# Performance work log

Hardware: AMD Instinct MI355X
Metric: run time of the kernel (lower is better)

## Reference

```python
import jax, jax.numpy as jnp
import numpy as np

N = 200000          # number of points (max_num_points // 2)
GRID = 0.4          # voxel edge length (meters)
NUM_BATCH = 4       # number of scenes encoded in points[:, 0]


def setup_inputs() -> dict:
    key = jax.random.key(0)
    k1, k2 = jax.random.split(key)
    xyz = jax.random.uniform(k1, (N, 3), minval=-50.0, maxval=50.0, dtype=jnp.float32)
    b = jax.random.randint(k2, (N,), 0, NUM_BATCH).astype(jnp.float32)
    points = jnp.concatenate([b[:, None], xyz], axis=1)  # [N, 4] = (batch, x, y, z)
    return {"points": points}


def reference(points):
    n = points.shape[0]
    vs = jnp.array([1.0, GRID, GRID, GRID], dtype=points.dtype)  # voxel_size
    decay2 = jnp.sum(vs[1:] ** 2) / 4.0  # decay_radius**2 = (||voxel_size||/2)**2

    pc_min = points.min(0) - vs * 2.0
    pc_max = points.max(0) + vs * 2.0
    coors = jnp.round((points - pc_min) / vs).astype(jnp.int32) + 1   # [N,4] voxel coords
    dims = (jnp.round((pc_max - pc_min) / vs) + 3.0).astype(jnp.int32)  # [4]

    def flatten(c):  # 4-D voxel coordinate -> 1-D hash key
        f = c[..., 0]
        for i in range(1, 4):
            f = f * dims[i] + c[..., i]
        return f

    keys = flatten(coors)  # [N]
    # unique occupied voxels (= query voxels); pad with max key so array stays sorted
    uq = jnp.unique(keys, size=n, fill_value=keys.max())  # [N] sorted
    valid = jnp.concatenate([jnp.array([True]), uq[1:] != uq[:-1]])  # first occurrence only

    # 27 spatial neighbor offsets ([0,-1,-1,-1]..[0,1,1,1]); batch offset is 0
    r = jnp.arange(-1, 2, dtype=jnp.int32)
    off = jnp.stack(jnp.meshgrid(r, r, r, indexing="ij"), -1).reshape(-1, 3)  # [27,3]
    off4 = jnp.concatenate([jnp.zeros((27, 1), jnp.int32), off], axis=1)      # [27,4]

    nb = coors[:, None, :] + off4[None, :, :]   # [N,27,4]: each point scatters to 27 query voxels
    nkeys = flatten(nb)                          # [N,27]
    idx = jnp.clip(jnp.searchsorted(uq, nkeys), 0, n - 1)
    hit = uq[idx] == nkeys                       # query voxel exists (is occupied)
    idx_safe = jnp.where(hit, idx, 0)

    # distance-decayed weight of point w.r.t. the query voxel center
    ctr = (nb[..., 1:].astype(points.dtype) - 1.0) * vs[1:] + pc_min[1:]  # [N,27,3]
    d2 = jnp.sum((points[:, None, 1:] - ctr) ** 2, axis=-1)               # [N,27]
    w = jnp.where(hit, jnp.exp(-d2 / decay2), 0.0)

    seg = lambda data: jax.ops.segment_sum(data, idx_safe.reshape(-1), num_segments=n)
    wf = w.reshape(-1)                               # [N*27]
    wsum = seg(wf)                                   # [M]
    p_rep = jnp.broadcast_to(points[:, None, :], (n, 27, 4)).reshape(-1, 4)
    wp = seg(wf[:, None] * p_rep)                    # [M,4] weighted first moment
    outer = points[:, 1:, None] * points[:, None, 1:]  # [N,3,3] xyz second moment
    o_rep = jnp.broadcast_to(outer[:, None], (n, 27, 3, 3)).reshape(-1, 3, 3)
    wo = seg(wf[:, None, None] * o_rep)              # [M,3,3]

    ok = valid & (wsum > 0)
    ws = jnp.where(ok, wsum, 1.0)
    mu = wp / ws[:, None]                            # [M,4] weighted mean (batch,x,y,z)
    sigma = wo / ws[:, None, None] - mu[:, 1:, None] * mu[:, None, 1:]  # weighted covariance
    sigma = (sigma + jnp.swapaxes(sigma, 1, 2)) / 2.0
    # padded / empty slots: well-conditioned placeholder with distinct singular values
    base = jnp.diag(jnp.array([3.0, 2.0, 1.0], dtype=points.dtype))
    sigma = jnp.where(ok[:, None, None], sigma, base)

    U, S, _ = jnp.linalg.svd(sigma)
    S = jnp.maximum(jnp.sqrt(S), 1e-6)
    flip = jnp.linalg.det(U) < 0
    col = jnp.where(flip, -1.0, 1.0)
    scale = jnp.stack([jnp.ones_like(col), jnp.ones_like(col), col], axis=-1)  # flip 3rd column
    R = (U * scale[:, None, :]) * S[:, None, :]

    mu = mu * ok[:, None]
    R = R * ok[:, None, None]
    return mu, R
```

## Files before the change

kernel.cpp:

```cpp
#include <hip/hip_runtime.h>
#include <stdint.h>


#define WMAX   5402624u
#define PBLK   2638
#define CHUNK  11
#define HCAP   1024
#define HITCAP 786432
#define MMB    784

struct Hdr {
  float pc_min[4];
  int   dims[4];
  int   M;
};

__device__ __forceinline__ unsigned fkey_map(float f) {
  unsigned u = __float_as_uint(f);
  return (u & 0x80000000u) ? ~u : (u | 0x80000000u);
}
__device__ __forceinline__ float fkey_unmap(unsigned u) {
  unsigned b = (u & 0x80000000u) ? (u ^ 0x80000000u) : ~u;
  return __uint_as_float(b);
}

__device__ __forceinline__ void coors_from(float4 p, float pc0, float pc1,
                                           float pc2, float pc3, int c[4]) {
  c[0] = (int)rintf((p.x - pc0) / 1.0f) + 1;
  c[1] = (int)rintf((p.y - pc1) / 0.4f) + 1;
  c[2] = (int)rintf((p.z - pc2) / 0.4f) + 1;
  c[3] = (int)rintf((p.w - pc3) / 0.4f) + 1;
}

__device__ __forceinline__ void direct_accum(float* __restrict__ acc, int r,
                                             float wgt, float4 p) {
  float* a = acc + (size_t)r * 12;
  atomicAdd((unsigned*)(a + 11), 1u);
  atomicAdd(a + 0, wgt);
  atomicAdd(a + 1, wgt * p.x);
  atomicAdd(a + 2, wgt * p.y);
  atomicAdd(a + 3, wgt * p.z);
  atomicAdd(a + 4, wgt * p.w);
  atomicAdd(a + 5, wgt * p.y * p.y);
  atomicAdd(a + 6, wgt * p.y * p.z);
  atomicAdd(a + 7, wgt * p.y * p.w);
  atomicAdd(a + 8, wgt * p.z * p.z);
  atomicAdd(a + 9, wgt * p.z * p.w);
  atomicAdd(a + 10, wgt * p.w * p.w);
}

__device__ __forceinline__ void jacobi_out(float ws, float4 v0, float4 v1,
                                           float4 v2, bool ok,
                                           float* mu_o, float* R_o) {
  if (!ok) {
    mu_o[0] = mu_o[1] = mu_o[2] = mu_o[3] = 0.0f;
    #pragma unroll
    for (int k = 0; k < 9; ++k) R_o[k] = 0.0f;
    return;
  }
  float mu0 = v0.y / ws, mu1 = v0.z / ws, mu2 = v0.w / ws, mu3 = v1.x / ws;
  float A[3][3];
  A[0][0] = v1.y / ws - mu1 * mu1;
  A[0][1] = A[1][0] = v1.z / ws - mu1 * mu2;
  A[0][2] = A[2][0] = v1.w / ws - mu1 * mu3;
  A[1][1] = v2.x / ws - mu2 * mu2;
  A[1][2] = A[2][1] = v2.y / ws - mu2 * mu3;
  A[2][2] = v2.z / ws - mu3 * mu3;

  float V[3][3] = {{1.f, 0.f, 0.f}, {0.f, 1.f, 0.f}, {0.f, 0.f, 1.f}};
  for (int sweep = 0; sweep < 8; ++sweep) {
    #pragma unroll
    for (int pi = 0; pi < 3; ++pi) {
      int p = (pi == 2) ? 1 : 0;
      int q = (pi == 0) ? 1 : 2;
      float apq = A[p][q];
      if (apq == 0.0f) continue;
      float app = A[p][p], aqq = A[q][q];
      float theta = (aqq - app) / (2.0f * apq);
      float t = 1.0f / (fabsf(theta) + sqrtf(theta * theta + 1.0f));
      if (theta < 0.0f) t = -t;
      float cth = 1.0f / sqrtf(t * t + 1.0f);
      float sth = t * cth;
      A[p][p] = app - t * apq;
      A[q][q] = aqq + t * apq;
      A[p][q] = A[q][p] = 0.0f;
      int k = 3 - p - q;
      float akp = A[k][p], akq = A[k][q];
      A[k][p] = A[p][k] = cth * akp - sth * akq;
      A[k][q] = A[q][k] = sth * akp + cth * akq;
      #pragma unroll
      for (int r = 0; r < 3; ++r) {
        float vp = V[r][p], vq = V[r][q];
        V[r][p] = cth * vp - sth * vq;
        V[r][q] = sth * vp + cth * vq;
      }
    }
  }
  float a[3] = {fabsf(A[0][0]), fabsf(A[1][1]), fabsf(A[2][2])};
  int idx[3] = {0, 1, 2};
  if (a[idx[0]] < a[idx[1]]) { int t = idx[0]; idx[0] = idx[1]; idx[1] = t; }
  if (a[idx[1]] < a[idx[2]]) { int t = idx[1]; idx[1] = idx[2]; idx[2] = t; }
  if (a[idx[0]] < a[idx[1]]) { int t = idx[0]; idx[0] = idx[1]; idx[1] = t; }
  float S0 = fmaxf(sqrtf(a[idx[0]]), 1e-6f);
  float S1 = fmaxf(sqrtf(a[idx[1]]), 1e-6f);
  float S2 = fmaxf(sqrtf(a[idx[2]]), 1e-6f);
  float U[3][3];
  #pragma unroll
  for (int r = 0; r < 3; ++r) {
    U[r][0] = V[r][idx[0]];
    U[r][1] = V[r][idx[1]];
    U[r][2] = V[r][idx[2]];
  }
  float det = U[0][0] * (U[1][1] * U[2][2] - U[1][2] * U[2][1])
            - U[0][1] * (U[1][0] * U[2][2] - U[1][2] * U[2][0])
            + U[0][2] * (U[1][0] * U[2][1] - U[1][1] * U[2][0]);
  float f2 = (det < 0.0f) ? -1.0f : 1.0f;
  mu_o[0] = mu0; mu_o[1] = mu1; mu_o[2] = mu2; mu_o[3] = mu3;
  R_o[0] = U[0][0] * S0; R_o[1] = U[0][1] * S1; R_o[2] = U[0][2] * S2 * f2;
  R_o[3] = U[1][0] * S0; R_o[4] = U[1][1] * S1; R_o[5] = U[1][2] * S2 * f2;
  R_o[6] = U[2][0] * S0; R_o[7] = U[2][1] * S1; R_o[8] = U[2][2] * S2 * f2;
}

__global__ void k_zero_minmax(const float4* __restrict__ pts, int n,
                              unsigned* __restrict__ mmpart,
                              unsigned* __restrict__ bm,
                              float* __restrict__ acc,
                              unsigned* __restrict__ g_cnt) {
  __shared__ unsigned smem[4 * 8];
  const int gtid = blockIdx.x * 256 + threadIdx.x;
  const int gridT = gridDim.x * 256;

  uint4 z = {0u, 0u, 0u, 0u};
  uint4* bm4 = (uint4*)bm;
  for (int i = gtid; i < (int)(WMAX / 4); i += gridT) bm4[i] = z;
  uint4* acc4 = (uint4*)acc;
  int acc4n = n * 3;
  for (int i = gtid; i < acc4n; i += gridT) acc4[i] = z;
  if (gtid == 0) *g_cnt = 0u;

  float mn[4] = { INFINITY,  INFINITY,  INFINITY,  INFINITY};
  float mx[4] = {-INFINITY, -INFINITY, -INFINITY, -INFINITY};
  for (int i = gtid; i < n; i += gridT) {
    float4 p = pts[i];
    mn[0] = fminf(mn[0], p.x); mx[0] = fmaxf(mx[0], p.x);
    mn[1] = fminf(mn[1], p.y); mx[1] = fmaxf(mx[1], p.y);
    mn[2] = fminf(mn[2], p.z); mx[2] = fmaxf(mx[2], p.z);
    mn[3] = fminf(mn[3], p.w); mx[3] = fmaxf(mx[3], p.w);
  }
  #pragma unroll
  for (int off = 32; off > 0; off >>= 1) {
    #pragma unroll
    for (int c = 0; c < 4; ++c) {
      mn[c] = fminf(mn[c], __shfl_down(mn[c], off));
      mx[c] = fmaxf(mx[c], __shfl_down(mx[c], off));
    }
  }
  int wave = threadIdx.x >> 6;
  if ((threadIdx.x & 63) == 0) {
    #pragma unroll
    for (int c = 0; c < 4; ++c) {
      smem[wave * 8 + c]     = fkey_map(mn[c]);
      smem[wave * 8 + 4 + c] = fkey_map(mx[c]);
    }
  }
  __syncthreads();
  int t = threadIdx.x;
  if (t < 8) {
    unsigned u = smem[t];
    #pragma unroll
    for (int w = 1; w < 4; ++w)
      u = (t < 4) ? min(u, smem[w * 8 + t]) : max(u, smem[w * 8 + t]);
    mmpart[blockIdx.x * 8 + t] = u;
  }
}

__global__ void k_prep(const unsigned* __restrict__ mmpart, Hdr* h, int nb) {
  __shared__ unsigned s[256 * 8];
  int t = threadIdx.x;
  unsigned v[8];
  #pragma unroll
  for (int c = 0; c < 4; ++c) { v[c] = 0xFFFFFFFFu; v[4 + c] = 0u; }
  for (int b = t; b < nb; b += 256) {
    #pragma unroll
    for (int c = 0; c < 4; ++c) {
      v[c] = min(v[c], mmpart[b * 8 + c]);
      v[4 + c] = max(v[4 + c], mmpart[b * 8 + 4 + c]);
    }
  }
  #pragma unroll
  for (int c = 0; c < 8; ++c) s[t * 8 + c] = v[c];
  __syncthreads();
  for (int off = 128; off > 0; off >>= 1) {
    if (t < off) {
      #pragma unroll
      for (int c = 0; c < 4; ++c)
        s[t * 8 + c] = min(s[t * 8 + c], s[(t + off) * 8 + c]);
      #pragma unroll
      for (int c = 4; c < 8; ++c)
        s[t * 8 + c] = max(s[t * 8 + c], s[(t + off) * 8 + c]);
    }
    __syncthreads();
  }
  if (t == 0) {
    const float vs[4] = {1.0f, 0.4f, 0.4f, 0.4f};
    #pragma unroll
    for (int c = 0; c < 4; ++c) {
      float mn = fkey_unmap(s[c]);
      float mx = fkey_unmap(s[4 + c]);
      float pmin = mn - vs[c] * 2.0f;
      float pmax = mx + vs[c] * 2.0f;
      h->pc_min[c] = pmin;
      h->dims[c] = (int)rintf((pmax - pmin) / vs[c]) + 3;
    }
  }
}

__global__ void k_mark(const float4* __restrict__ pts, int n,
                       const Hdr* __restrict__ h, unsigned* __restrict__ bm) {
  int i = blockIdx.x * 256 + threadIdx.x;
  if (i >= n) return;
  float4 p = pts[i];
  int c[4];
  coors_from(p, h->pc_min[0], h->pc_min[1], h->pc_min[2], h->pc_min[3], c);
  int key = ((c[0] * h->dims[1] + c[1]) * h->dims[2] + c[2]) * h->dims[3] + c[3];
  unsigned uk = (unsigned)key;
  if (uk >= WMAX * 32u) return;
  atomicOr(&bm[uk >> 5], 1u << (uk & 31u));
}

__global__ void k_scanA(const unsigned* __restrict__ bm,
                        unsigned short* __restrict__ rank16,
                        unsigned* __restrict__ part) {
  __shared__ unsigned s[256];
  int t = threadIdx.x;
  size_t base = (size_t)blockIdx.x * 2048 + (size_t)t * 8;
  uint4 a = *(const uint4*)(bm + base);
  uint4 b = *(const uint4*)(bm + base + 4);
  unsigned pc[8] = {(unsigned)__popc(a.x), (unsigned)__popc(a.y),
                    (unsigned)__popc(a.z), (unsigned)__popc(a.w),
                    (unsigned)__popc(b.x), (unsigned)__popc(b.y),
                    (unsigned)__popc(b.z), (unsigned)__popc(b.w)};
  unsigned sum = 0;
  #pragma unroll
  for (int k = 0; k < 8; ++k) sum += pc[k];
  s[t] = sum; __syncthreads();
  for (int off = 1; off < 256; off <<= 1) {
    unsigned v = (t >= off) ? s[t - off] : 0u;
    __syncthreads();
    s[t] += v;
    __syncthreads();
  }
  unsigned run = s[t] - sum;
  unsigned r[8];
  #pragma unroll
  for (int k = 0; k < 8; ++k) { r[k] = run; run += pc[k]; }
  uint4 o;
  o.x = (r[0] & 0xFFFFu) | (r[1] << 16);
  o.y = (r[2] & 0xFFFFu) | (r[3] << 16);
  o.z = (r[4] & 0xFFFFu) | (r[5] << 16);
  o.w = (r[6] & 0xFFFFu) | (r[7] << 16);
  *(uint4*)(rank16 + base) = o;
  if (t == 255) part[blockIdx.x] = s[255];
}

__global__ void k_scanB(unsigned* __restrict__ part, Hdr* h) {
  __shared__ unsigned s[256];
  int t = threadIdx.x;
  int lo = t * CHUNK;
  unsigned local[CHUNK];
  unsigned sum = 0;
  #pragma unroll
  for (int k = 0; k < CHUNK; ++k) {
    int j = lo + k;
    local[k] = (j < PBLK) ? part[j] : 0u;
    sum += local[k];
  }
  s[t] = sum; __syncthreads();
  for (int off = 1; off < 256; off <<= 1) {
    unsigned v = (t >= off) ? s[t - off] : 0u;
    __syncthreads();
    s[t] += v;
    __syncthreads();
  }
  unsigned run = s[t] - sum;
  #pragma unroll
  for (int k = 0; k < CHUNK; ++k) {
    int j = lo + k;
    if (j < PBLK) part[j] = run;
    run += local[k];
  }
  if (t == 255) h->M = (int)s[255];
}

__global__ void k_probe(const float4* __restrict__ pts, int n,
                        const Hdr* __restrict__ h,
                        const unsigned* __restrict__ bm,
                        const unsigned short* __restrict__ rank16,
                        const unsigned* __restrict__ part,
                        int* __restrict__ hit_i, int* __restrict__ hit_r,
                        float* __restrict__ hit_w,
                        unsigned* __restrict__ g_cnt,
                        float* __restrict__ acc) {
  __shared__ int s_cnt;
  __shared__ int s_base;
  __shared__ int   s_i[HCAP];
  __shared__ int   s_r[HCAP];
  __shared__ float s_w[HCAP];
  if (threadIdx.x == 0) s_cnt = 0;
  __syncthreads();
  int i = blockIdx.x * 256 + threadIdx.x;
  const float gg = 0.4f * 0.4f;
  const float decay2 = (gg + gg + gg) * 0.25f;
  if (i < n) {
    float4 p = pts[i];
    int c[4];
    coors_from(p, h->pc_min[0], h->pc_min[1], h->pc_min[2], h->pc_min[3], c);
    int d1 = h->dims[1], d2 = h->dims[2], d3 = h->dims[3];
    float m1 = h->pc_min[1], m2 = h->pc_min[2], m3 = h->pc_min[3];
    #pragma unroll
    for (int dx = -1; dx <= 1; ++dx) {
      #pragma unroll
      for (int dy = -1; dy <= 1; ++dy) {
        int n1 = c[1] + dx, n2 = c[2] + dy;
        int kc = ((c[0] * d1 + n1) * d2 + n2) * d3 + c[3];
        unsigned k = (unsigned)kc;
        if (k < 1u || k + 1u >= WMAX * 32u) continue;
        unsigned w = k >> 5, b = k & 31u;
        unsigned cur = bm[w];
        unsigned tri;
        if (b == 0u)
          tri = (bm[w - 1] >> 31) | ((cur & 3u) << 1);
        else if (b == 31u)
          tri = ((cur >> 30) & 3u) | ((bm[w + 1] & 1u) << 2);
        else
          tri = (cur >> (b - 1)) & 7u;
        if (!tri) continue;
        #pragma unroll
        for (int j = 0; j < 3; ++j) {
          if (!((tri >> j) & 1u)) continue;
          unsigned kj = k + (unsigned)(j - 1);
          unsigned wj = kj >> 5, bj = kj & 31u;
          unsigned word = (wj == w) ? cur : bm[wj];
          int r = (int)(part[kj >> 16] + (unsigned)rank16[wj] +
                        __popc(word & ((1u << bj) - 1u)));
          int n3 = c[3] + (j - 1);
          float cx = (float)(n1 - 1) * 0.4f + m1;
          float cy = (float)(n2 - 1) * 0.4f + m2;
          float cz = (float)(n3 - 1) * 0.4f + m3;
          float ex = p.y - cx, ey = p.z - cy, ez = p.w - cz;
          float dd = ex * ex + ey * ey + ez * ez;
          float wgt = expf(-dd / decay2);
          int pos = atomicAdd(&s_cnt, 1);
          if (pos < HCAP) {
            s_i[pos] = i; s_r[pos] = r; s_w[pos] = wgt;
          } else {
            direct_accum(acc, r, wgt, p);
          }
        }
      }
    }
  }
  __syncthreads();
  int cnt = min(s_cnt, HCAP);
  if (threadIdx.x == 0) s_base = (int)atomicAdd(g_cnt, (unsigned)cnt);
  __syncthreads();
  int base = s_base;
  for (int j = threadIdx.x; j < cnt; j += 256) {
    int gpos = base + j;
    int r = s_r[j];
    if (gpos < HITCAP) {
      hit_i[gpos] = s_i[j];
      hit_r[gpos] = r;
      hit_w[gpos] = s_w[j];
      atomicAdd((unsigned*)(acc + (size_t)r * 12 + 11), 1u);
    } else {
      direct_accum(acc, r, s_w[j], pts[s_i[j]]);
    }
  }
}

__global__ void k_drain(const float4* __restrict__ pts,
                        const int* __restrict__ hit_i,
                        const int* __restrict__ hit_r,
                        const float* __restrict__ hit_w,
                        const unsigned* __restrict__ g_cnt,
                        float* __restrict__ acc) {
  int total = min((int)*g_cnt, HITCAP);
  for (int j = blockIdx.x * 256 + threadIdx.x; j < total;
       j += gridDim.x * 256) {
    int r = hit_r[j];
    float wgt = hit_w[j];
    float4 q = pts[hit_i[j]];
    float* a = acc + (size_t)r * 12;
    unsigned c = *(const unsigned*)(a + 11);
    if (c == 1u) {
      float4 v0 = {wgt, wgt * q.x, wgt * q.y, wgt * q.z};
      float4 v1 = {wgt * q.w, wgt * q.y * q.y, wgt * q.y * q.z,
                   wgt * q.y * q.w};
      float4 v2 = {wgt * q.z * q.z, wgt * q.z * q.w, wgt * q.w * q.w, 0.0f};
      float4* av = (float4*)a;
      av[0] = v0; av[1] = v1; av[2] = v2;
    } else {
      atomicAdd(a + 0, wgt);
      atomicAdd(a + 1, wgt * q.x);
      atomicAdd(a + 2, wgt * q.y);
      atomicAdd(a + 3, wgt * q.z);
      atomicAdd(a + 4, wgt * q.w);
      atomicAdd(a + 5, wgt * q.y * q.y);
      atomicAdd(a + 6, wgt * q.y * q.z);
      atomicAdd(a + 7, wgt * q.y * q.w);
      atomicAdd(a + 8, wgt * q.z * q.z);
      atomicAdd(a + 9, wgt * q.z * q.w);
      atomicAdd(a + 10, wgt * q.w * q.w);
    }
  }
}

__global__ void k_finalize(const Hdr* __restrict__ h,
                           const float* __restrict__ acc,
                           float* __restrict__ out_mu,
                           float* __restrict__ out_R, int n) {
  int i = blockIdx.x * 256 + threadIdx.x;
  if (i >= n) return;
  const float4* av = (const float4*)(acc + (size_t)i * 12);
  float4 v0 = av[0], v1 = av[1], v2 = av[2];
  float ws = v0.x;
  bool ok = (i < h->M) && (ws > 0.0f);
  jacobi_out(ws, v0, v1, v2, ok, out_mu + (size_t)i * 4,
             out_R + (size_t)i * 9);
}

extern "C" void kernel_launch(void* const* d_in, const int* in_sizes, int n_in,
                              void* d_out, int out_size, void* d_ws,
                              size_t ws_size, hipStream_t stream) {
  const float4* pts = (const float4*)d_in[0];
  int n = in_sizes[0] / 4;
  float* out = (float*)d_out;
  float* outR = out + (size_t)4 * n;

  char* ws = (char*)d_ws;
  Hdr* hdr = (Hdr*)ws;
  size_t off = 256;
  unsigned* mmpart = (unsigned*)(ws + off);      off += (size_t)MMB * 8 * 4;
  unsigned* bm = (unsigned*)(ws + off);          off += (size_t)WMAX * 4;
  unsigned short* rank16 = (unsigned short*)(ws + off); off += (size_t)WMAX * 2;
  unsigned* part = (unsigned*)(ws + off);        off += 4096 * 4;
  unsigned* g_cnt = (unsigned*)(ws + off);       off += 256;
  int* hit_i = (int*)(ws + off);                 off += (size_t)HITCAP * 4;
  int* hit_r = (int*)(ws + off);                 off += (size_t)HITCAP * 4;
  float* hit_w = (float*)(ws + off);             off += (size_t)HITCAP * 4;
  float* acc = (float*)(ws + off);
  size_t needed = off + (size_t)n * 12 * 4;
  if (ws_size < needed) return;

  int nb = (n + 255) / 256;
  k_zero_minmax<<<MMB, 256, 0, stream>>>(pts, n, mmpart, bm, acc, g_cnt);
  k_prep<<<1, 256, 0, stream>>>(mmpart, hdr, MMB);
  k_mark<<<nb, 256, 0, stream>>>(pts, n, hdr, bm);
  k_scanA<<<PBLK, 256, 0, stream>>>(bm, rank16, part);
  k_scanB<<<1, 256, 0, stream>>>(part, hdr);
  k_probe<<<nb, 256, 0, stream>>>(pts, n, hdr, bm, rank16, part,
                                  hit_i, hit_r, hit_w, g_cnt, acc);
  k_drain<<<512, 256, 0, stream>>>(pts, hit_i, hit_r, hit_w, g_cnt, acc);
  k_finalize<<<nb, 256, 0, stream>>>(hdr, acc, out, outR, n);
}
```

Measured before the change: 176.8 us.

## Restrict bitmap zero/scan to occupied key range, add coarse occupancy bitmap, fuse scans

Computes the range of scan blocks that the batch-coordinate span can actually touch and zeroes and scans only that part of the voxel bitmap instead of the whole buffer. Adds a byte-level coarse bitmap so probes skip loads of empty bitmap words. Merges the two scan kernels with a last-block-done counter, splits min/max from zeroing, and writes the single-point voxel output directly in the drain kernel, so finalize skips those voxels. In exchange it adds an extra coarse-bitmap lookup per probe and relies on atomic completion ordering. It also changes the single-point result to mu equal to the point and R equal to 1e-6 times the identity, which may differ from the reference weighted mean.

```diff
diff --git a/kernel.cpp b/kernel.cpp
--- a/kernel.cpp
+++ b/kernel.cpp
@@ -7,12 +7,12 @@
 #define CHUNK  11
 #define HCAP   1024
 #define HITCAP 786432
-#define MMB    784
 
 struct Hdr {
   float pc_min[4];
   int   dims[4];
   int   M;
+  int   sb_lo, sb_hi;
 };
 
 __device__ __forceinline__ unsigned fkey_map(float f) {
@@ -35,7 +35,7 @@
 __device__ __forceinline__ void direct_accum(float* __restrict__ acc, int r,
                                              float wgt, float4 p) {
   float* a = acc + (size_t)r * 12;
-  atomicAdd((unsigned*)(a + 11), 1u);
+  atomicAdd((unsigned*)(a + 11), 2u);
   atomicAdd(a + 0, wgt);
   atomicAdd(a + 1, wgt * p.x);
   atomicAdd(a + 2, wgt * p.y);
@@ -50,14 +50,7 @@
 }
 
 __device__ __forceinline__ void jacobi_out(float ws, float4 v0, float4 v1,
-                                           float4 v2, bool ok,
-                                           float* mu_o, float* R_o) {
-  if (!ok) {
-    mu_o[0] = mu_o[1] = mu_o[2] = mu_o[3] = 0.0f;
-    #pragma unroll
-    for (int k = 0; k < 9; ++k) R_o[k] = 0.0f;
-    return;
-  }
+                                           float4 v2, float* mu_o, float* R_o) {
   float mu0 = v0.y / ws, mu1 = v0.z / ws, mu2 = v0.w / ws, mu3 = v1.x / ws;
   float A[3][3];
   A[0][0] = v1.y / ws - mu1 * mu1;
@@ -121,26 +114,13 @@
   R_o[6] = U[2][0] * S0; R_o[7] = U[2][1] * S1; R_o[8] = U[2][2] * S2 * f2;
 }
 
-__global__ void k_zero_minmax(const float4* __restrict__ pts, int n,
-                              unsigned* __restrict__ mmpart,
-                              unsigned* __restrict__ bm,
-                              float* __restrict__ acc,
-                              unsigned* __restrict__ g_cnt) {
+__global__ void k_minmax(const float4* __restrict__ pts, int n,
+                         unsigned* __restrict__ mmpart) {
   __shared__ unsigned smem[4 * 8];
-  const int gtid = blockIdx.x * 256 + threadIdx.x;
-  const int gridT = gridDim.x * 256;
-
-  uint4 z = {0u, 0u, 0u, 0u};
-  uint4* bm4 = (uint4*)bm;
-  for (int i = gtid; i < (int)(WMAX / 4); i += gridT) bm4[i] = z;
-  uint4* acc4 = (uint4*)acc;
-  int acc4n = n * 3;
-  for (int i = gtid; i < acc4n; i += gridT) acc4[i] = z;
-  if (gtid == 0) *g_cnt = 0u;
-
   float mn[4] = { INFINITY,  INFINITY,  INFINITY,  INFINITY};
   float mx[4] = {-INFINITY, -INFINITY, -INFINITY, -INFINITY};
-  for (int i = gtid; i < n; i += gridT) {
+  for (int i = blockIdx.x * blockDim.x + threadIdx.x; i < n;
+       i += gridDim.x * blockDim.x) {
     float4 p = pts[i];
     mn[0] = fminf(mn[0], p.x); mx[0] = fmaxf(mx[0], p.x);
     mn[1] = fminf(mn[1], p.y); mx[1] = fmaxf(mx[1], p.y);
@@ -212,7 +192,43 @@
       h->pc_min[c] = pmin;
       h->dims[c] = (int)rintf((pmax - pmin) / vs[c]) + 3;
     }
-  }
+    float min0 = fkey_unmap(s[0]);
+    float max0 = fkey_unmap(s[4]);
+    int c0min = (int)rintf(min0 - h->pc_min[0]) + 1;
+    int c0max = (int)rintf(max0 - h->pc_min[0]) + 1;
+    long long D = (long long)h->dims[1] * h->dims[2] * h->dims[3];
+    long long keylo = (long long)c0min * D;
+    long long keyhi = (long long)(c0max + 1) * D;
+    int sblo = 0, sbhi = PBLK;
+    if (keylo >= 0 && keyhi <= (long long)WMAX * 32ll) {
+      sblo = max(0, (int)((keylo >> 5) >> 11) - 1);
+      sbhi = min((int)PBLK, (int)((((keyhi + 31) >> 5) + 2047) >> 11) + 1);
+    }
+    h->sb_lo = sblo;
+    h->sb_hi = sbhi;
+  }
+}
+
+__global__ void k_zero(const Hdr* __restrict__ h, unsigned* __restrict__ bm,
+                       unsigned char* __restrict__ cb, float* __restrict__ acc,
+                       unsigned* __restrict__ part,
+                       unsigned* __restrict__ g_cnt,
+                       unsigned* __restrict__ scan_done, int n) {
+  const int gtid = blockIdx.x * 256 + threadIdx.x;
+  const int gridT = gridDim.x * 256;
+  size_t wlo = (size_t)h->sb_lo << 11, whi = (size_t)h->sb_hi << 11;
+  uint4 z = {0u, 0u, 0u, 0u};
+  uint4* b4 = (uint4*)(bm + wlo);
+  int nb4 = (int)((whi - wlo) >> 2);
+  for (int i = gtid; i < nb4; i += gridT) b4[i] = z;
+  uint4* c4 = (uint4*)(cb + (wlo >> 3));
+  int nc4 = (int)((whi - wlo) >> 7);
+  for (int i = gtid; i < nc4; i += gridT) c4[i] = z;
+  uint4* a4 = (uint4*)acc;
+  int na4 = n * 3;
+  for (int i = gtid; i < na4; i += gridT) a4[i] = z;
+  for (int i = gtid; i < 4096; i += gridT) part[i] = 0u;
+  if (gtid == 0) { *g_cnt = 0u; *scan_done = 0u; }
 }
 
 __global__ void k_mark(const float4* __restrict__ pts, int n,
@@ -228,21 +244,64 @@
   atomicOr(&bm[uk >> 5], 1u << (uk & 31u));
 }
 
-__global__ void k_scanA(const unsigned* __restrict__ bm,
-                        unsigned short* __restrict__ rank16,
-                        unsigned* __restrict__ part) {
+__global__ void k_scanAB(const unsigned* __restrict__ bm,
+                         unsigned short* __restrict__ rank16,
+                         unsigned char* __restrict__ cb,
+                         unsigned* __restrict__ part,
+                         unsigned* __restrict__ scan_done, Hdr* h) {
   __shared__ unsigned s[256];
+  __shared__ int s_last;
   int t = threadIdx.x;
-  size_t base = (size_t)blockIdx.x * 2048 + (size_t)t * 8;
-  uint4 a = *(const uint4*)(bm + base);
-  uint4 b = *(const uint4*)(bm + base + 4);
-  unsigned pc[8] = {(unsigned)__popc(a.x), (unsigned)__popc(a.y),
-                    (unsigned)__popc(a.z), (unsigned)__popc(a.w),
-                    (unsigned)__popc(b.x), (unsigned)__popc(b.y),
-                    (unsigned)__popc(b.z), (unsigned)__popc(b.w)};
+  int vb = blockIdx.x;
+  if (vb >= h->sb_lo && vb < h->sb_hi) {
+    size_t base = (size_t)vb * 2048 + (size_t)t * 8;
+    uint4 a = *(const uint4*)(bm + base);
+    uint4 b = *(const uint4*)(bm + base + 4);
+    unsigned wv[8] = {a.x, a.y, a.z, a.w, b.x, b.y, b.z, b.w};
+    unsigned pc[8], sum = 0, cbyte = 0;
+    #pragma unroll
+    for (int k = 0; k < 8; ++k) {
+      pc[k] = (unsigned)__popc(wv[k]);
+      sum += pc[k];
+      cbyte |= (wv[k] != 0u ? 1u : 0u) << k;
+    }
+    cb[(size_t)vb * 256 + t] = (unsigned char)cbyte;
+    s[t] = sum; __syncthreads();
+    for (int off = 1; off < 256; off <<= 1) {
+      unsigned v = (t >= off) ? s[t - off] : 0u;
+      __syncthreads();
+      s[t] += v;
+      __syncthreads();
+    }
+    unsigned run = s[t] - sum;
+    unsigned r[8];
+    #pragma unroll
+    for (int k = 0; k < 8; ++k) { r[k] = run; run += pc[k]; }
+    uint4 o;
+    o.x = (r[0] & 0xFFFFu) | (r[1] << 16);
+    o.y = (r[2] & 0xFFFFu) | (r[3] << 16);
+    o.z = (r[4] & 0xFFFFu) | (r[5] << 16);
+    o.w = (r[6] & 0xFFFFu) | (r[7] << 16);
+    *(uint4*)(rank16 + base) = o;
+    if (t == 255) part[vb] = s[255];
+  }
+  __syncthreads();
+  if (t == 0) {
+    __threadfence();
+    unsigned old = atomicAdd(scan_done, 1u);
+    s_last = (old == gridDim.x - 1u) ? 1 : 0;
+  }
+  __syncthreads();
+  if (!s_last) return;
+  int lo = t * CHUNK;
+  unsigned local[CHUNK];
   unsigned sum = 0;
   #pragma unroll
-  for (int k = 0; k < 8; ++k) sum += pc[k];
+  for (int k = 0; k < CHUNK; ++k) {
+    int j = lo + k;
+    local[k] = (j < PBLK) ? atomicAdd(&part[j], 0u) : 0u;
+    sum += local[k];
+  }
   s[t] = sum; __syncthreads();
   for (int off = 1; off < 256; off <<= 1) {
     unsigned v = (t >= off) ? s[t - off] : 0u;
@@ -251,38 +310,6 @@
     __syncthreads();
   }
   unsigned run = s[t] - sum;
-  unsigned r[8];
-  #pragma unroll
-  for (int k = 0; k < 8; ++k) { r[k] = run; run += pc[k]; }
-  uint4 o;
-  o.x = (r[0] & 0xFFFFu) | (r[1] << 16);
-  o.y = (r[2] & 0xFFFFu) | (r[3] << 16);
-  o.z = (r[4] & 0xFFFFu) | (r[5] << 16);
-  o.w = (r[6] & 0xFFFFu) | (r[7] << 16);
-  *(uint4*)(rank16 + base) = o;
-  if (t == 255) part[blockIdx.x] = s[255];
-}
-
-__global__ void k_scanB(unsigned* __restrict__ part, Hdr* h) {
-  __shared__ unsigned s[256];
-  int t = threadIdx.x;
-  int lo = t * CHUNK;
-  unsigned local[CHUNK];
-  unsigned sum = 0;
-  #pragma unroll
-  for (int k = 0; k < CHUNK; ++k) {
-    int j = lo + k;
-    local[k] = (j < PBLK) ? part[j] : 0u;
-    sum += local[k];
-  }
-  s[t] = sum; __syncthreads();
-  for (int off = 1; off < 256; off <<= 1) {
-    unsigned v = (t >= off) ? s[t - off] : 0u;
-    __syncthreads();
-    s[t] += v;
-    __syncthreads();
-  }
-  unsigned run = s[t] - sum;
   #pragma unroll
   for (int k = 0; k < CHUNK; ++k) {
     int j = lo + k;
@@ -292,9 +319,12 @@
   if (t == 255) h->M = (int)s[255];
 }
 
+#define CBIT(x) ((cb[(x) >> 3] >> ((x) & 7u)) & 1u)
+
 __global__ void k_probe(const float4* __restrict__ pts, int n,
                         const Hdr* __restrict__ h,
                         const unsigned* __restrict__ bm,
+                        const unsigned char* __restrict__ cb,
                         const unsigned short* __restrict__ rank16,
                         const unsigned* __restrict__ part,
                         int* __restrict__ hit_i, int* __restrict__ hit_r,
@@ -326,21 +356,25 @@
         unsigned k = (unsigned)kc;
         if (k < 1u || k + 1u >= WMAX * 32u) continue;
         unsigned w = k >> 5, b = k & 31u;
-        unsigned cur = bm[w];
-        unsigned tri;
-        if (b == 0u)
-          tri = (bm[w - 1] >> 31) | ((cur & 3u) << 1);
-        else if (b == 31u)
-          tri = ((cur >> 30) & 3u) | ((bm[w + 1] & 1u) << 2);
-        else
-          tri = (cur >> (b - 1)) & 7u;
+        unsigned tri = 0;
+        if (b != 0u && b != 31u) {
+          if (CBIT(w)) tri = (bm[w] >> (b - 1)) & 7u;
+        } else if (b == 0u) {
+          unsigned t0 = CBIT(w - 1) ? (bm[w - 1] >> 31) : 0u;
+          unsigned t1 = CBIT(w) ? ((bm[w] & 3u) << 1) : 0u;
+          tri = t0 | t1;
+        } else {
+          unsigned t0 = CBIT(w) ? ((bm[w] >> 30) & 3u) : 0u;
+          unsigned t1 = CBIT(w + 1) ? ((bm[w + 1] & 1u) << 2) : 0u;
+          tri = t0 | t1;
+        }
         if (!tri) continue;
         #pragma unroll
         for (int j = 0; j < 3; ++j) {
           if (!((tri >> j) & 1u)) continue;
           unsigned kj = k + (unsigned)(j - 1);
           unsigned wj = kj >> 5, bj = kj & 31u;
-          unsigned word = (wj == w) ? cur : bm[wj];
+          unsigned word = bm[wj];
           int r = (int)(part[kj >> 16] + (unsigned)rank16[wj] +
                         __popc(word & ((1u << bj) - 1u)));
           int n3 = c[3] + (j - 1);
@@ -384,7 +418,9 @@
                         const int* __restrict__ hit_r,
                         const float* __restrict__ hit_w,
                         const unsigned* __restrict__ g_cnt,
-                        float* __restrict__ acc) {
+                        float* __restrict__ acc,
+                        float* __restrict__ out_mu,
+                        float* __restrict__ out_R) {
   int total = min((int)*g_cnt, HITCAP);
   for (int j = blockIdx.x * 256 + threadIdx.x; j < total;
        j += gridDim.x * 256) {
@@ -394,12 +430,11 @@
     float* a = acc + (size_t)r * 12;
     unsigned c = *(const unsigned*)(a + 11);
     if (c == 1u) {
-      float4 v0 = {wgt, wgt * q.x, wgt * q.y, wgt * q.z};
-      float4 v1 = {wgt * q.w, wgt * q.y * q.y, wgt * q.y * q.z,
-                   wgt * q.y * q.w};
-      float4 v2 = {wgt * q.z * q.z, wgt * q.z * q.w, wgt * q.w * q.w, 0.0f};
-      float4* av = (float4*)a;
-      av[0] = v0; av[1] = v1; av[2] = v2;
+      *(float4*)(out_mu + (size_t)r * 4) = q;
+      float* R_o = out_R + (size_t)r * 9;
+      R_o[0] = 1e-6f; R_o[1] = 0.f;   R_o[2] = 0.f;
+      R_o[3] = 0.f;   R_o[4] = 1e-6f; R_o[5] = 0.f;
+      R_o[6] = 0.f;   R_o[7] = 0.f;   R_o[8] = 1e-6f;
     } else {
       atomicAdd(a + 0, wgt);
       atomicAdd(a + 1, wgt * q.x);
@@ -422,12 +457,19 @@
                            float* __restrict__ out_R, int n) {
   int i = blockIdx.x * 256 + threadIdx.x;
   if (i >= n) return;
+  float* mu_o = out_mu + (size_t)i * 4;
+  float* R_o = out_R + (size_t)i * 9;
+  if (i >= h->M) {
+    mu_o[0] = mu_o[1] = mu_o[2] = mu_o[3] = 0.0f;
+    #pragma unroll
+    for (int k = 0; k < 9; ++k) R_o[k] = 0.0f;
+    return;
+  }
   const float4* av = (const float4*)(acc + (size_t)i * 12);
+  unsigned c = *(const unsigned*)(acc + (size_t)i * 12 + 11);
+  if (c == 1u) return;
   float4 v0 = av[0], v1 = av[1], v2 = av[2];
-  float ws = v0.x;
-  bool ok = (i < h->M) && (ws > 0.0f);
-  jacobi_out(ws, v0, v1, v2, ok, out_mu + (size_t)i * 4,
-             out_R + (size_t)i * 9);
+  jacobi_out(v0.x, v0, v1, v2, mu_o, R_o);
 }
 
 extern "C" void kernel_launch(void* const* d_in, const int* in_sizes, int n_in,
@@ -441,11 +483,13 @@
   char* ws = (char*)d_ws;
   Hdr* hdr = (Hdr*)ws;
   size_t off = 256;
-  unsigned* mmpart = (unsigned*)(ws + off);      off += (size_t)MMB * 8 * 4;
+  unsigned* mmpart = (unsigned*)(ws + off);      off += 256 * 8 * 4;
   unsigned* bm = (unsigned*)(ws + off);          off += (size_t)WMAX * 4;
   unsigned short* rank16 = (unsigned short*)(ws + off); off += (size_t)WMAX * 2;
+  unsigned char* cb = (unsigned char*)(ws + off); off += (size_t)(WMAX / 8) + 256;
   unsigned* part = (unsigned*)(ws + off);        off += 4096 * 4;
-  unsigned* g_cnt = (unsigned*)(ws + off);       off += 256;
+  unsigned* g_cnt = (unsigned*)(ws + off);       off += 128;
+  unsigned* scan_done = (unsigned*)(ws + off);   off += 128;
   int* hit_i = (int*)(ws + off);                 off += (size_t)HITCAP * 4;
   int* hit_r = (int*)(ws + off);                 off += (size_t)HITCAP * 4;
   float* hit_w = (float*)(ws + off);             off += (size_t)HITCAP * 4;
@@ -454,13 +498,14 @@
   if (ws_size < needed) return;
 
   int nb = (n + 255) / 256;
-  k_zero_minmax<<<MMB, 256, 0, stream>>>(pts, n, mmpart, bm, acc, g_cnt);
-  k_prep<<<1, 256, 0, stream>>>(mmpart, hdr, MMB);
+  k_minmax<<<256, 256, 0, stream>>>(pts, n, mmpart);
+  k_prep<<<1, 256, 0, stream>>>(mmpart, hdr, 256);
+  k_zero<<<784, 256, 0, stream>>>(hdr, bm, cb, acc, part, g_cnt, scan_done, n);
   k_mark<<<nb, 256, 0, stream>>>(pts, n, hdr, bm);
-  k_scanA<<<PBLK, 256, 0, stream>>>(bm, rank16, part);
-  k_scanB<<<1, 256, 0, stream>>>(part, hdr);
-  k_probe<<<nb, 256, 0, stream>>>(pts, n, hdr, bm, rank16, part,
+  k_scanAB<<<PBLK, 256, 0, stream>>>(bm, rank16, cb, part, scan_done, hdr);
+  k_probe<<<nb, 256, 0, stream>>>(pts, n, hdr, bm, cb, rank16, part,
                                   hit_i, hit_r, hit_w, g_cnt, acc);
-  k_drain<<<512, 256, 0, stream>>>(pts, hit_i, hit_r, hit_w, g_cnt, acc);
+  k_drain<<<512, 256, 0, stream>>>(pts, hit_i, hit_r, hit_w, g_cnt, acc,
+                                   out, outR);
   k_finalize<<<nb, 256, 0, stream>>>(hdr, acc, out, outR, n);
 }
```

Measured after the change: 244.0 us. +38.0%, slower.

## Restrict bitmap scan to occupied key range and streamline Jacobi finalize

Applied to the files above, without the earlier changes.

Computes in k_prep the range of bitmap super-blocks that can contain keys, from the batch-coordinate min/max. k_scanA then returns early for blocks outside that range, with partial sums pre-zeroed. The Jacobi eigen-solver is rewritten with scalar registers and a fully unrolled sweep loop, and the ok-branch moves to finalize, keyed on M. Count bookkeeping is changed so that slots never written read as weight zero. Skipped blocks leave rank16 uninitialised, which relies on probes never reading outside the range.

```diff
diff --git a/kernel.cpp b/kernel.cpp
--- a/kernel.cpp
+++ b/kernel.cpp
@@ -13,6 +13,7 @@
   float pc_min[4];
   int   dims[4];
   int   M;
+  int   sb_lo, sb_hi;
 };
 
 __device__ __forceinline__ unsigned fkey_map(float f) {
@@ -35,7 +36,7 @@
 __device__ __forceinline__ void direct_accum(float* __restrict__ acc, int r,
                                              float wgt, float4 p) {
   float* a = acc + (size_t)r * 12;
-  atomicAdd((unsigned*)(a + 11), 1u);
+  atomicAdd((unsigned*)(a + 11), 2u);
   atomicAdd(a + 0, wgt);
   atomicAdd(a + 1, wgt * p.x);
   atomicAdd(a + 2, wgt * p.y);
@@ -49,82 +50,86 @@
   atomicAdd(a + 10, wgt * p.w * p.w);
 }
 
+__device__ __forceinline__ void jrot(float& app, float& aqq, float& apq,
+                                     float& akp, float& akq,
+                                     float& vp0, float& vp1, float& vp2,
+                                     float& vq0, float& vq1, float& vq2) {
+  float a = apq;
+  if (a == 0.0f) return;
+  float theta = (aqq - app) / (2.0f * a);
+  float t = 1.0f / (fabsf(theta) + sqrtf(theta * theta + 1.0f));
+  if (theta < 0.0f) t = -t;
+  float c = 1.0f / sqrtf(t * t + 1.0f);
+  float s = t * c;
+  app -= t * a;
+  aqq += t * a;
+  apq = 0.0f;
+  float kp = akp, kq = akq;
+  akp = c * kp - s * kq;
+  akq = s * kp + c * kq;
+  float x, y;
+  x = vp0; y = vq0; vp0 = c * x - s * y; vq0 = s * x + c * y;
+  x = vp1; y = vq1; vp1 = c * x - s * y; vq1 = s * x + c * y;
+  x = vp2; y = vq2; vp2 = c * x - s * y; vq2 = s * x + c * y;
+}
+
 __device__ __forceinline__ void jacobi_out(float ws, float4 v0, float4 v1,
-                                           float4 v2, bool ok,
-                                           float* mu_o, float* R_o) {
-  if (!ok) {
-    mu_o[0] = mu_o[1] = mu_o[2] = mu_o[3] = 0.0f;
-    #pragma unroll
-    for (int k = 0; k < 9; ++k) R_o[k] = 0.0f;
-    return;
-  }
+                                           float4 v2, float* mu_o, float* R_o) {
   float mu0 = v0.y / ws, mu1 = v0.z / ws, mu2 = v0.w / ws, mu3 = v1.x / ws;
-  float A[3][3];
-  A[0][0] = v1.y / ws - mu1 * mu1;
-  A[0][1] = A[1][0] = v1.z / ws - mu1 * mu2;
-  A[0][2] = A[2][0] = v1.w / ws - mu1 * mu3;
-  A[1][1] = v2.x / ws - mu2 * mu2;
-  A[1][2] = A[2][1] = v2.y / ws - mu2 * mu3;
-  A[2][2] = v2.z / ws - mu3 * mu3;
-
-  float V[3][3] = {{1.f, 0.f, 0.f}, {0.f, 1.f, 0.f}, {0.f, 0.f, 1.f}};
+  float a00 = v1.y / ws - mu1 * mu1;
+  float a01 = v1.z / ws - mu1 * mu2;
+  float a02 = v1.w / ws - mu1 * mu3;
+  float a11 = v2.x / ws - mu2 * mu2;
+  float a12 = v2.y / ws - mu2 * mu3;
+  float a22 = v2.z / ws - mu3 * mu3;
+
+  float u00 = 1.f, u01 = 0.f, u02 = 0.f;
+  float u10 = 0.f, u11 = 1.f, u12 = 0.f;
+  float u20 = 0.f, u21 = 0.f, u22 = 1.f;
+  #pragma unroll
   for (int sweep = 0; sweep < 8; ++sweep) {
-    #pragma unroll
-    for (int pi = 0; pi < 3; ++pi) {
-      int p = (pi == 2) ? 1 : 0;
-      int q = (pi == 0) ? 1 : 2;
-      float apq = A[p][q];
-      if (apq == 0.0f) continue;
-      float app = A[p][p], aqq = A[q][q];
-      float theta = (aqq - app) / (2.0f * apq);
-      float t = 1.0f / (fabsf(theta) + sqrtf(theta * theta + 1.0f));
-      if (theta < 0.0f) t = -t;
-      float cth = 1.0f / sqrtf(t * t + 1.0f);
-      float sth = t * cth;
-      A[p][p] = app - t * apq;
-      A[q][q] = aqq + t * apq;
-      A[p][q] = A[q][p] = 0.0f;
-      int k = 3 - p - q;
-      float akp = A[k][p], akq = A[k][q];
-      A[k][p] = A[p][k] = cth * akp - sth * akq;
-      A[k][q] = A[q][k] = sth * akp + cth * akq;
-      #pragma unroll
-      for (int r = 0; r < 3; ++r) {
-        float vp = V[r][p], vq = V[r][q];
-        V[r][p] = cth * vp - sth * vq;
-        V[r][q] = sth * vp + cth * vq;
-      }
-    }
-  }
-  float a[3] = {fabsf(A[0][0]), fabsf(A[1][1]), fabsf(A[2][2])};
-  int idx[3] = {0, 1, 2};
-  if (a[idx[0]] < a[idx[1]]) { int t = idx[0]; idx[0] = idx[1]; idx[1] = t; }
-  if (a[idx[1]] < a[idx[2]]) { int t = idx[1]; idx[1] = idx[2]; idx[2] = t; }
-  if (a[idx[0]] < a[idx[1]]) { int t = idx[0]; idx[0] = idx[1]; idx[1] = t; }
-  float S0 = fmaxf(sqrtf(a[idx[0]]), 1e-6f);
-  float S1 = fmaxf(sqrtf(a[idx[1]]), 1e-6f);
-  float S2 = fmaxf(sqrtf(a[idx[2]]), 1e-6f);
-  float U[3][3];
-  #pragma unroll
-  for (int r = 0; r < 3; ++r) {
-    U[r][0] = V[r][idx[0]];
-    U[r][1] = V[r][idx[1]];
-    U[r][2] = V[r][idx[2]];
-  }
-  float det = U[0][0] * (U[1][1] * U[2][2] - U[1][2] * U[2][1])
-            - U[0][1] * (U[1][0] * U[2][2] - U[1][2] * U[2][0])
-            + U[0][2] * (U[1][0] * U[2][1] - U[1][1] * U[2][0]);
-  float f2 = (det < 0.0f) ? -1.0f : 1.0f;
+    jrot(a00, a11, a01, a02, a12, u00, u10, u20, u01, u11, u21);
+    jrot(a00, a22, a02, a01, a12, u00, u10, u20, u02, u12, u22);
+    jrot(a11, a22, a12, a01, a02, u01, u11, u21, u02, u12, u22);
+  }
+  float l0 = fabsf(a00), l1 = fabsf(a11), l2 = fabsf(a22);
+  float t;
+  if (l0 < l1) {
+    t = l0; l0 = l1; l1 = t;
+    t = u00; u00 = u01; u01 = t;
+    t = u10; u10 = u11; u11 = t;
+    t = u20; u20 = u21; u21 = t;
+  }
+  if (l1 < l2) {
+    t = l1; l1 = l2; l2 = t;
+    t = u01; u01 = u02; u02 = t;
+    t = u11; u11 = u12; u12 = t;
+    t = u21; u21 = u22; u22 = t;
+  }
+  if (l0 < l1) {
+    t = l0; l0 = l1; l1 = t;
+    t = u00; u00 = u01; u01 = t;
+    t = u10; u10 = u11; u11 = t;
+    t = u20; u20 = u21; u21 = t;
+  }
+  float S0 = fmaxf(sqrtf(l0), 1e-6f);
+  float S1 = fmaxf(sqrtf(l1), 1e-6f);
+  float S2 = fmaxf(sqrtf(l2), 1e-6f);
+  float det = u00 * (u11 * u22 - u12 * u21)
+            - u01 * (u10 * u22 - u12 * u20)
+            + u02 * (u10 * u21 - u11 * u20);
+  float f2 = (det < 0.0f) ? -S2 : S2;
   mu_o[0] = mu0; mu_o[1] = mu1; mu_o[2] = mu2; mu_o[3] = mu3;
-  R_o[0] = U[0][0] * S0; R_o[1] = U[0][1] * S1; R_o[2] = U[0][2] * S2 * f2;
-  R_o[3] = U[1][0] * S0; R_o[4] = U[1][1] * S1; R_o[5] = U[1][2] * S2 * f2;
-  R_o[6] = U[2][0] * S0; R_o[7] = U[2][1] * S1; R_o[8] = U[2][2] * S2 * f2;
+  R_o[0] = u00 * S0; R_o[1] = u01 * S1; R_o[2] = u02 * f2;
+  R_o[3] = u10 * S0; R_o[4] = u11 * S1; R_o[5] = u12 * f2;
+  R_o[6] = u20 * S0; R_o[7] = u21 * S1; R_o[8] = u22 * f2;
 }
 
 __global__ void k_zero_minmax(const float4* __restrict__ pts, int n,
                               unsigned* __restrict__ mmpart,
                               unsigned* __restrict__ bm,
                               float* __restrict__ acc,
+                              unsigned* __restrict__ part,
                               unsigned* __restrict__ g_cnt) {
   __shared__ unsigned smem[4 * 8];
   const int gtid = blockIdx.x * 256 + threadIdx.x;
@@ -136,6 +141,7 @@
   uint4* acc4 = (uint4*)acc;
   int acc4n = n * 3;
   for (int i = gtid; i < acc4n; i += gridT) acc4[i] = z;
+  for (int i = gtid; i < 4096; i += gridT) part[i] = 0u;
   if (gtid == 0) *g_cnt = 0u;
 
   float mn[4] = { INFINITY,  INFINITY,  INFINITY,  INFINITY};
@@ -212,6 +218,20 @@
       h->pc_min[c] = pmin;
       h->dims[c] = (int)rintf((pmax - pmin) / vs[c]) + 3;
     }
+    float min0 = fkey_unmap(s[0]);
+    float max0 = fkey_unmap(s[4]);
+    int c0min = (int)rintf(min0 - h->pc_min[0]) + 1;
+    int c0max = (int)rintf(max0 - h->pc_min[0]) + 1;
+    long long D = (long long)h->dims[1] * h->dims[2] * h->dims[3];
+    long long keylo = (long long)c0min * D;
+    long long keyhi = (long long)(c0max + 1) * D;
+    int sblo = 0, sbhi = PBLK;
+    if (keylo >= 0 && keyhi <= (long long)WMAX * 32ll) {
+      sblo = max(0, (int)((keylo >> 5) >> 11) - 1);
+      sbhi = min((int)PBLK, (int)((((keyhi + 31) >> 5) + 2047) >> 11) + 1);
+    }
+    h->sb_lo = sblo;
+    h->sb_hi = sbhi;
   }
 }
 
@@ -230,10 +250,13 @@
 
 __global__ void k_scanA(const unsigned* __restrict__ bm,
                         unsigned short* __restrict__ rank16,
-                        unsigned* __restrict__ part) {
+                        unsigned* __restrict__ part,
+                        const Hdr* __restrict__ h) {
   __shared__ unsigned s[256];
   int t = threadIdx.x;
-  size_t base = (size_t)blockIdx.x * 2048 + (size_t)t * 8;
+  int vb = blockIdx.x;
+  if (vb < h->sb_lo || vb >= h->sb_hi) return;
+  size_t base = (size_t)vb * 2048 + (size_t)t * 8;
   uint4 a = *(const uint4*)(bm + base);
   uint4 b = *(const uint4*)(bm + base + 4);
   unsigned pc[8] = {(unsigned)__popc(a.x), (unsigned)__popc(a.y),
@@ -260,7 +283,7 @@
   o.z = (r[4] & 0xFFFFu) | (r[5] << 16);
   o.w = (r[6] & 0xFFFFu) | (r[7] << 16);
   *(uint4*)(rank16 + base) = o;
-  if (t == 255) part[blockIdx.x] = s[255];
+  if (t == 255) part[vb] = s[255];
 }
 
 __global__ void k_scanB(unsigned* __restrict__ part, Hdr* h) {
@@ -397,7 +420,8 @@
       float4 v0 = {wgt, wgt * q.x, wgt * q.y, wgt * q.z};
       float4 v1 = {wgt * q.w, wgt * q.y * q.y, wgt * q.y * q.z,
                    wgt * q.y * q.w};
-      float4 v2 = {wgt * q.z * q.z, wgt * q.z * q.w, wgt * q.w * q.w, 0.0f};
+      float4 v2 = {wgt * q.z * q.z, wgt * q.z * q.w, wgt * q.w * q.w,
+                   __uint_as_float(1u)};
       float4* av = (float4*)a;
       av[0] = v0; av[1] = v1; av[2] = v2;
     } else {
@@ -422,12 +446,17 @@
                            float* __restrict__ out_R, int n) {
   int i = blockIdx.x * 256 + threadIdx.x;
   if (i >= n) return;
+  float* mu_o = out_mu + (size_t)i * 4;
+  float* R_o = out_R + (size_t)i * 9;
+  if (i >= h->M) {
+    mu_o[0] = mu_o[1] = mu_o[2] = mu_o[3] = 0.0f;
+    #pragma unroll
+    for (int k = 0; k < 9; ++k) R_o[k] = 0.0f;
+    return;
+  }
   const float4* av = (const float4*)(acc + (size_t)i * 12);
   float4 v0 = av[0], v1 = av[1], v2 = av[2];
-  float ws = v0.x;
-  bool ok = (i < h->M) && (ws > 0.0f);
-  jacobi_out(ws, v0, v1, v2, ok, out_mu + (size_t)i * 4,
-             out_R + (size_t)i * 9);
+  jacobi_out(v0.x, v0, v1, v2, mu_o, R_o);
 }
 
 extern "C" void kernel_launch(void* const* d_in, const int* in_sizes, int n_in,
@@ -454,10 +483,10 @@
   if (ws_size < needed) return;
 
   int nb = (n + 255) / 256;
-  k_zero_minmax<<<MMB, 256, 0, stream>>>(pts, n, mmpart, bm, acc, g_cnt);
+  k_zero_minmax<<<MMB, 256, 0, stream>>>(pts, n, mmpart, bm, acc, part, g_cnt);
   k_prep<<<1, 256, 0, stream>>>(mmpart, hdr, MMB);
   k_mark<<<nb, 256, 0, stream>>>(pts, n, hdr, bm);
-  k_scanA<<<PBLK, 256, 0, stream>>>(bm, rank16, part);
+  k_scanA<<<PBLK, 256, 0, stream>>>(bm, rank16, part, hdr);
   k_scanB<<<1, 256, 0, stream>>>(part, hdr);
   k_probe<<<nb, 256, 0, stream>>>(pts, n, hdr, bm, rank16, part,
                                   hit_i, hit_r, hit_w, g_cnt, acc);
```

Result: faster. 161.3 us (-8.8%).
